# Kernel tuning notes

Measured on AMD Instinct MI355X. Metric: run time of the kernel, lower is better.

## Reference

```python
import jax, jax.numpy as jnp
import numpy as np

B, S, D, F, E, TOP_K = 2, 2048, 1024, 2048, 8, 2


def setup_inputs() -> dict:
    key = jax.random.key(0)
    k0, k1, k2, k3 = jax.random.split(key, 4)
    return {
        "hidden_states": jax.random.normal(k0, (B, S, D), jnp.float32),
        "gate_w": jax.random.normal(k1, (E, D), jnp.float32) * 0.02,   # torch Linear weight [out=E, in=D]
        "w1": jax.random.normal(k2, (E, D, F), jnp.float32) * 0.02,    # per-expert up-proj
        "w2": jax.random.normal(k3, (E, F, D), jnp.float32) * 0.02,    # per-expert down-proj
    }


def reference(hidden_states, gate_w, w1, w2):
    b, s, d = hidden_states.shape
    e = gate_w.shape[0]
    x = hidden_states.reshape(-1, d)                 # [T, D]
    t = x.shape[0]
    router_logits = x @ gate_w.T                     # [T, E]
    # softmax in fp32 as in original, then renormalized top-k weights
    probs = jax.nn.softmax(router_logits.astype(jnp.float32), axis=-1)
    topw, sel = jax.lax.top_k(probs, TOP_K)          # [T, K]
    topw = topw / jnp.sum(topw, axis=-1, keepdims=True)
    topw = topw.astype(x.dtype)
    # dense combine weights: zero for unselected experts (top_k indices are distinct)
    combine = jnp.zeros((t, e), x.dtype).at[jnp.arange(t)[:, None], sel].add(topw)  # [T, E]
    out = jnp.zeros_like(x)
    for ei in range(e):  # small fixed expert count
        h = jax.nn.silu(x @ w1[ei]) @ w2[ei]         # [T, D]
        out = out + combine[:, ei:ei + 1] * h
    return out.reshape(b, s, d), router_logits
```

## Files before the change

### kernel.cpp

```cpp
#include <hip/hip_runtime.h>
#include <hip/hip_bf16.h>
#include <math.h>

#define Tt 4096
#define Dd 1024
#define Ff 2048
#define Ee 8

typedef unsigned short u16;
typedef short bf16x8 __attribute__((ext_vector_type(8)));
typedef float f32x4 __attribute__((ext_vector_type(4)));

__device__ __forceinline__ u16 f2bf(float f) {
  union { float f; unsigned u; } v; v.f = f;
  unsigned r = v.u + 0x7fffu + ((v.u >> 16) & 1u);
  return (u16)(r >> 16);
}

__device__ __forceinline__ void gload16(const void* g, void* l) {
  __builtin_amdgcn_global_load_lds(
      (const __attribute__((address_space(1))) unsigned int*)g,
      (__attribute__((address_space(3))) unsigned int*)l, 16, 0, 0);
}

__device__ __forceinline__ void router_body(
    int t, int tid, const float* __restrict__ x, const float* __restrict__ gw,
    float* __restrict__ logits, u16* __restrict__ xb)
{
  int lane = tid & 63;
  const float* xr = x + (size_t)t * Dd;
  float xv[16];
#pragma unroll
  for (int i = 0; i < 4; ++i) {
    float4 v = *reinterpret_cast<const float4*>(xr + lane * 16 + i * 4);
    xv[i*4+0] = v.x; xv[i*4+1] = v.y; xv[i*4+2] = v.z; xv[i*4+3] = v.w;
  }
  if (xb) {
#pragma unroll
    for (int i = 0; i < 4; ++i) {
      ushort4 b;
      b.x = f2bf(xv[i*4+0]); b.y = f2bf(xv[i*4+1]);
      b.z = f2bf(xv[i*4+2]); b.w = f2bf(xv[i*4+3]);
      *reinterpret_cast<ushort4*>(xb + (size_t)t * Dd + lane * 16 + i * 4) = b;
    }
  }
#pragma unroll
  for (int e = 0; e < Ee; ++e) {
    const float* gr = gw + (size_t)e * Dd + lane * 16;
    float s = 0.f;
#pragma unroll
    for (int i = 0; i < 4; ++i) {
      float4 g = *reinterpret_cast<const float4*>(gr + i * 4);
      s += xv[i*4+0]*g.x + xv[i*4+1]*g.y + xv[i*4+2]*g.z + xv[i*4+3]*g.w;
    }
#pragma unroll
    for (int o = 32; o > 0; o >>= 1) s += __shfl_xor(s, o);
    if (lane == 0) logits[(size_t)t * Ee + e] = s;
  }
}

__device__ __forceinline__ void top2_of(
    const float* __restrict__ logits, int t, int& i1, int& i2, float& wa)
{
  float4 lo = *reinterpret_cast<const float4*>(logits + (size_t)t * 8);
  float4 hi = *reinterpret_cast<const float4*>(logits + (size_t)t * 8 + 4);
  float s[8] = {lo.x, lo.y, lo.z, lo.w, hi.x, hi.y, hi.z, hi.w};
  i1 = 0; float m1 = s[0];
#pragma unroll
  for (int e = 1; e < 8; ++e) if (s[e] > m1) { m1 = s[e]; i1 = e; }
  i2 = -1; float m2 = -__builtin_inff();
#pragma unroll
  for (int e = 0; e < 8; ++e) if (e != i1 && s[e] > m2) { m2 = s[e]; i2 = e; }
  wa = 1.f / (1.f + expf(m2 - m1));
}

__device__ __forceinline__ void transpose_tile(
    const float* __restrict__ ip, u16* __restrict__ op, int R, int C,
    int r0, int c0, int tid, u16 st[][65])
{
  int rr = tid >> 2;
  int cb = (tid & 3) * 16;
#pragma unroll
  for (int i = 0; i < 4; ++i) {
    float4 v = *reinterpret_cast<const float4*>(ip + (size_t)(r0 + rr) * C + c0 + cb + i * 4);
    st[rr][cb + i*4 + 0] = f2bf(v.x);
    st[rr][cb + i*4 + 1] = f2bf(v.y);
    st[rr][cb + i*4 + 2] = f2bf(v.z);
    st[rr][cb + i*4 + 3] = f2bf(v.w);
  }
  __syncthreads();
#pragma unroll
  for (int i = 0; i < 4; ++i) {
    ushort4 b;
    b.x = st[cb + i*4 + 0][rr];
    b.y = st[cb + i*4 + 1][rr];
    b.z = st[cb + i*4 + 2][rr];
    b.w = st[cb + i*4 + 3][rr];
    *reinterpret_cast<ushort4*>(op + (size_t)(c0 + rr) * R + r0 + cb + i * 4) = b;
  }
}

template<int MODE, int N_, int K_>
__device__ __forceinline__ void gemm_body(
    int orig, u16* __restrict__ Al, u16* __restrict__ Bl,
    const u16* __restrict__ Abase, const u16* __restrict__ Bbase,
    void* __restrict__ Cout, const int* __restrict__ meta,
    const int* __restrict__ list, const float* __restrict__ wgt)
{
  constexpr int NXc = N_ / 128;
  constexpr int NYc = 32;
  constexpr int CPX = NXc * NYc;
  constexpr int ABUF = 128 * 32;
  constexpr int NT  = K_ / 32;

  const int swz  = (orig & 7) * CPX + (orig >> 3);
  const int bz   = swz / CPX;
  const int rem  = swz - bz * CPX;
  const int by   = rem / NXc;
  const int bx   = rem - by * NXc;

  const int e   = bz;
  const int cnt = meta[e];
  if (by * 128 >= cnt) return;
  const int off = meta[32 + e];

  const int tid  = threadIdx.x;
  const int lane = tid & 63;
  const int wave = tid >> 6;
  const int wr   = wave >> 1, wc = wave & 1;
  const int n0   = bx * 128;

  const int l4 = lane >> 2;
  const int kp = (((lane & 3) ^ ((lane >> 3) & 3))) * 8;

  const u16* aptr[2];
  int aoff[2];
#pragma unroll
  for (int c = 0; c < 2; ++c) {
    int chunk = wave * 2 + c;
    int row = chunk * 16 + l4;
    int i = by * 128 + row;
    if (i >= cnt) i = cnt - 1;
    int srow = (MODE == 0) ? list[off + i] : (off + i);
    aptr[c] = Abase + (size_t)srow * K_ + kp;
    aoff[c] = chunk * 512;
  }
  const u16* bptr[2];
  int boff[2];
#pragma unroll
  for (int c = 0; c < 2; ++c) {
    int chunk = wave * 2 + c;
    int row = chunk * 16 + l4;
    bptr[c] = Bbase + ((size_t)e * N_ + n0 + row) * K_ + kp;
    boff[c] = chunk * 512;
  }

  f32x4 acc[4][4] = {};
  const int r16 = lane & 15;
  const int kqs = (((lane >> 4) ^ ((lane >> 1) & 3))) * 8;

  u16 *a0 = Al, *a1 = Al + ABUF, *a2 = Al + 2 * ABUF;
  u16 *b0 = Bl, *b1 = Bl + ABUF, *b2 = Bl + 2 * ABUF;

#pragma unroll
  for (int c = 0; c < 2; ++c) { gload16(aptr[c], a0 + aoff[c]); gload16(bptr[c], b0 + boff[c]); }
#pragma unroll
  for (int c = 0; c < 2; ++c) { gload16(aptr[c] + 32, a1 + aoff[c]); gload16(bptr[c] + 32, b1 + boff[c]); }

  for (int t = 0; t < NT; ++t) {
    if (t + 1 < NT) asm volatile("s_waitcnt vmcnt(4)" ::: "memory");
    else            asm volatile("s_waitcnt vmcnt(0)" ::: "memory");
    __builtin_amdgcn_s_barrier();

    if (t + 2 < NT) {
      int k0 = (t + 2) * 32;
#pragma unroll
      for (int c = 0; c < 2; ++c) { gload16(aptr[c] + k0, a2 + aoff[c]); gload16(bptr[c] + k0, b2 + boff[c]); }
    }

    bf16x8 af[4], bfv[4];
#pragma unroll
    for (int m = 0; m < 4; ++m)
      af[m] = *reinterpret_cast<const bf16x8*>(&a0[(wr*64 + m*16 + r16) * 32 + kqs]);
#pragma unroll
    for (int n = 0; n < 4; ++n)
      bfv[n] = *reinterpret_cast<const bf16x8*>(&b0[(wc*64 + n*16 + r16) * 32 + kqs]);
    __builtin_amdgcn_s_setprio(1);
#pragma unroll
    for (int m = 0; m < 4; ++m)
#pragma unroll
      for (int n = 0; n < 4; ++n)
        acc[m][n] = __builtin_amdgcn_mfma_f32_16x16x32_bf16(af[m], bfv[n], acc[m][n], 0, 0, 0);
    __builtin_amdgcn_s_setprio(0);

    u16* ta = a0; a0 = a1; a1 = a2; a2 = ta;
    u16* tb = b0; b0 = b1; b1 = b2; b2 = tb;
  }

  const int colb = n0 + wc * 64 + r16;
  const int rb4  = wr * 64 + ((lane >> 4) << 2);
#pragma unroll
  for (int m = 0; m < 4; ++m) {
#pragma unroll
    for (int r = 0; r < 4; ++r) {
      int i = by * 128 + rb4 + m * 16 + r;
      if (i >= cnt) continue;
      if (MODE == 0) {
        u16* hp = (u16*)Cout + (size_t)(off + i) * N_;
#pragma unroll
        for (int n = 0; n < 4; ++n) {
          float v = acc[m][n][r];
          v = v / (1.f + expf(-v));
          hp[colb + n * 16] = f2bf(v);
        }
      } else {
        int   tok = list[off + i];
        float w   = wgt[off + i];
        float* o = (float*)Cout + (size_t)tok * N_;
#pragma unroll
        for (int n = 0; n < 4; ++n)
          atomicAdd(&o[colb + n * 16], w * acc[m][n][r]);
      }
    }
  }
}

__global__ __launch_bounds__(256) void router_kernel(
    const float* __restrict__ x, const float* __restrict__ gw,
    float* __restrict__ logits, u16* __restrict__ xb)
{
  router_body(blockIdx.x * 4 + (threadIdx.x >> 6), threadIdx.x, x, gw, logits, xb);
}

__global__ __launch_bounds__(256) void fuse1_kernel(
    const float* __restrict__ x, const float* __restrict__ gw,
    float* __restrict__ logits, u16* __restrict__ xb,
    const float* __restrict__ w1, u16* __restrict__ w1T,
    float* __restrict__ outz)
{
  __shared__ u16 st[64][65];
  const int orig = blockIdx.x;
  if (orig < 4096) {
    int swz = (orig & 7) * 512 + (orig >> 3);
    int e   = swz / 512;
    int rem = swz - e * 512;
    int by  = rem / 32, bx = rem - (rem / 32) * 32;
    const size_t eo = (size_t)e * Dd * Ff;
    transpose_tile(w1 + eo, w1T + eo, Dd, Ff, by * 64, bx * 64, threadIdx.x, st);
  } else if (orig < 5120) {
    router_body((orig - 4096) * 4 + (threadIdx.x >> 6), threadIdx.x, x, gw, logits, xb);
  } else {
    int z = orig - 5120;
    float4 zero = make_float4(0.f, 0.f, 0.f, 0.f);
    float4* p = reinterpret_cast<float4*>(outz);
#pragma unroll
    for (int i = 0; i < 16; ++i)
      p[(size_t)z * 4096 + i * 256 + threadIdx.x] = zero;
  }
}

__global__ __launch_bounds__(256) void fuse2_kernel(
    const u16* __restrict__ Abase, const u16* __restrict__ Bbase,
    void* __restrict__ Cout, const int* __restrict__ meta,
    const int* __restrict__ list, const float* __restrict__ wgt,
    const float* __restrict__ w2, u16* __restrict__ w2T)
{
  constexpr int ABUF = 128 * 32;
  __shared__ u16 pool[6 * ABUF];
  const int orig = blockIdx.x;
  if (orig < 4096) {
    gemm_body<0, Ff, Dd>(orig, pool, pool + 3 * ABUF, Abase, Bbase, Cout, meta, list, wgt);
  } else {
    int og  = orig - 4096;
    int swz = (og & 7) * 512 + (og >> 3);
    int e   = swz / 512;
    int rem = swz - e * 512;
    int byy = rem / 16, bxx = rem - (rem / 16) * 16;
    const size_t eo = (size_t)e * Ff * Dd;
    transpose_tile(w2 + eo, w2T + eo, Ff, Dd, byy * 64, bxx * 64, threadIdx.x,
                   reinterpret_cast<u16(*)[65]>(pool));
  }
}

template<int MODE, int N_, int K_>
__global__ __launch_bounds__(256) void gemm_g(
    const u16* __restrict__ Abase, const u16* __restrict__ Bbase,
    void* __restrict__ Cout, const int* __restrict__ meta,
    const int* __restrict__ list, const float* __restrict__ wgt)
{
  constexpr int ABUF = 128 * 32;
  __shared__ u16 Al[3 * ABUF];
  __shared__ u16 Bl[3 * ABUF];
  const int orig = blockIdx.x + (N_ / 128) * (blockIdx.y + 32 * blockIdx.z);
  gemm_body<MODE, N_, K_>(orig, Al, Bl, Abase, Bbase, Cout, meta, list, wgt);
}

__global__ __launch_bounds__(256) void transpose_bf16_kernel(
    const float* __restrict__ in, u16* __restrict__ out, int R, int C)
{
  __shared__ u16 st[64][65];
  const size_t eoff = (size_t)blockIdx.z * R * C;
  transpose_tile(in + eoff, out + eoff, R, C, blockIdx.y * 64, blockIdx.x * 64,
                 threadIdx.x, st);
}

__global__ __launch_bounds__(256) void build1_kernel(
    const float* __restrict__ logits, int* __restrict__ meta)
{
  __shared__ int cnt;
  const int e = blockIdx.x;
  const int tid = threadIdx.x;
  if (tid == 0) cnt = 0;
  __syncthreads();
  int local = 0;
  for (int it = 0; it < Tt / 256; ++it) {
    int t = it * 256 + tid;
    int i1, i2; float wa;
    top2_of(logits, t, i1, i2, wa);
    if (i1 == e || i2 == e) ++local;
  }
  atomicAdd(&cnt, local);
  __syncthreads();
  if (tid == 0) meta[e] = cnt;
}

__global__ __launch_bounds__(256) void build2_kernel(
    const float* __restrict__ logits, int* __restrict__ meta,
    int* __restrict__ list, float* __restrict__ wgt)
{
  __shared__ int cur;
  const int e = blockIdx.x;
  const int tid = threadIdx.x;
  int offv = 0;
  if (tid == 0) {
    for (int g = 0; g < Ee; ++g) { if (g < e) offv += meta[g]; }
    meta[32 + e] = offv;
    cur = 0;
  }
  __syncthreads();
  offv = meta[32 + e];
  for (int it = 0; it < Tt / 256; ++it) {
    int t = it * 256 + tid;
    int i1, i2; float wa;
    top2_of(logits, t, i1, i2, wa);
    float w = (i1 == e) ? wa : ((i2 == e) ? (1.f - wa) : 0.f);
    if (i1 == e || i2 == e) {
      int pos = atomicAdd(&cur, 1);
      list[offv + pos] = t;
      wgt[offv + pos] = w;
    }
  }
}

__global__ __launch_bounds__(256) void combine_kernel(
    const float* __restrict__ logits, float* __restrict__ combine)
{
  int t = blockIdx.x * 256 + threadIdx.x;
  if (t >= Tt) return;
  int i1, i2; float wa;
  top2_of(logits, t, i1, i2, wa);
#pragma unroll
  for (int e = 0; e < 8; ++e)
    combine[(size_t)t * 8 + e] = (e == i1) ? wa : ((e == i2) ? (1.f - wa) : 0.f);
}

template<int MODE, int N_, int K_>
__global__ __launch_bounds__(256) void gemm_dense(
    const float* __restrict__ A, const float* __restrict__ Bg,
    float* __restrict__ C, const float* __restrict__ combine,
    int expert, int first)
{
  constexpr int BM = 128, BN = 128, BK = 32, LDT = 40;
  __shared__ u16 Al[BM * LDT];
  __shared__ u16 Bl[BN * LDT];
  const int tid  = threadIdx.x;
  const int lane = tid & 63;
  const int wave = tid >> 6;
  const int wr = wave >> 1, wc = wave & 1;
  const int m0 = blockIdx.y * BM;
  const int n0 = blockIdx.x * BN;
  f32x4 acc[4][4] = {};
  for (int k0 = 0; k0 < K_; k0 += BK) {
#pragma unroll
    for (int i = 0; i < 4; ++i) {
      int f = tid + 256 * i;
      int row = f >> 3;
      int c4 = (f & 7) << 2;
      float4 v = *reinterpret_cast<const float4*>(A + (size_t)(m0 + row) * K_ + k0 + c4);
      ushort4 b;
      b.x = f2bf(v.x); b.y = f2bf(v.y); b.z = f2bf(v.z); b.w = f2bf(v.w);
      *reinterpret_cast<ushort4*>(&Al[row * LDT + c4]) = b;
    }
    {
      int n  = tid & 127;
      int kb = (tid >> 7) << 4;
      const float* bp = Bg + (size_t)(k0 + kb) * N_ + n0 + n;
      u16 tmp[16];
#pragma unroll
      for (int kk = 0; kk < 16; ++kk)
        tmp[kk] = f2bf(bp[(size_t)kk * N_]);
      u16* p = &Bl[n * LDT + kb];
#pragma unroll
      for (int i = 0; i < 4; ++i) {
        ushort4 b;
        b.x = tmp[i*4+0]; b.y = tmp[i*4+1]; b.z = tmp[i*4+2]; b.w = tmp[i*4+3];
        *reinterpret_cast<ushort4*>(p + i * 4) = b;
      }
    }
    __syncthreads();
    bf16x8 af[4], bfr[4];
    const int kq  = (lane >> 4) << 3;
    const int r16 = lane & 15;
#pragma unroll
    for (int m = 0; m < 4; ++m)
      af[m] = *reinterpret_cast<const bf16x8*>(&Al[(wr*64 + m*16 + r16) * LDT + kq]);
#pragma unroll
    for (int n = 0; n < 4; ++n)
      bfr[n] = *reinterpret_cast<const bf16x8*>(&Bl[(wc*64 + n*16 + r16) * LDT + kq]);
#pragma unroll
    for (int m = 0; m < 4; ++m)
#pragma unroll
      for (int n = 0; n < 4; ++n)
        acc[m][n] = __builtin_amdgcn_mfma_f32_16x16x32_bf16(af[m], bfr[n], acc[m][n], 0, 0, 0);
    __syncthreads();
  }
  const int col0 = n0 + wc * 64 + (lane & 15);
  const int rbs  = m0 + wr * 64 + ((lane >> 4) << 2);
#pragma unroll
  for (int m = 0; m < 4; ++m) {
#pragma unroll
    for (int r = 0; r < 4; ++r) {
      int row = rbs + m * 16 + r;
      if (MODE == 0) {
#pragma unroll
        for (int n = 0; n < 4; ++n) {
          float v = acc[m][n][r];
          v = v / (1.f + expf(-v));
          C[(size_t)row * N_ + col0 + n * 16] = v;
        }
      } else {
        float w = combine[(size_t)row * Ee + expert];
        if (first) {
#pragma unroll
          for (int n = 0; n < 4; ++n)
            C[(size_t)row * N_ + col0 + n * 16] = w * acc[m][n][r];
        } else {
#pragma unroll
          for (int n = 0; n < 4; ++n)
            C[(size_t)row * N_ + col0 + n * 16] += w * acc[m][n][r];
        }
      }
    }
  }
}

extern "C" void kernel_launch(void* const* d_in, const int* in_sizes, int n_in,
                              void* d_out, int out_size, void* d_ws, size_t ws_size,
                              hipStream_t stream)
{
  const float* x  = (const float*)d_in[0];
  const float* gw = (const float*)d_in[1];
  const float* w1 = (const float*)d_in[2];
  const float* w2 = (const float*)d_in[3];
  float* out    = (float*)d_out;
  float* logits = out + (size_t)Tt * Dd;

  int*   meta = (int*)d_ws;
  int*   list = (int*)((char*)d_ws + 256);
  float* wgt  = (float*)((char*)d_ws + 256 + 32768);
  u16*   xb   = (u16*)((char*)d_ws + 262144);
  u16*   h1   = (u16*)((char*)d_ws + 262144 + 8388608);
  u16*   wA   = (u16*)((char*)d_ws + 262144 + 8388608 + 33554432);
  u16*   wB   = (u16*)((char*)d_ws + 262144 + 8388608 + 2*33554432ull);
  const size_t NEED_B = 262144ull + 8388608ull + 33554432ull + 33554432ull;
  const size_t NEED_A = NEED_B + 33554432ull;

  if (ws_size >= NEED_B) {
    fuse1_kernel<<<5376, 256, 0, stream>>>(x, gw, logits, xb, w1, wA, out);
    build1_kernel<<<Ee, 256, 0, stream>>>(logits, meta);
    build2_kernel<<<Ee, 256, 0, stream>>>(logits, meta, list, wgt);
    if (ws_size >= NEED_A) {
      fuse2_kernel<<<8192, 256, 0, stream>>>(xb, wA, h1, meta, list, wgt, w2, wB);
      gemm_g<1, Dd, Ff><<<dim3(Dd/128, 32, 8), 256, 0, stream>>>(h1, wB, out, meta, list, wgt);
    } else {
      gemm_g<0, Ff, Dd><<<dim3(Ff/128, 32, 8), 256, 0, stream>>>(xb, wA, h1, meta, list, wgt);
      transpose_bf16_kernel<<<dim3(Dd/64, Ff/64, Ee), 256, 0, stream>>>(w2, wA, Ff, Dd);
      gemm_g<1, Dd, Ff><<<dim3(Dd/128, 32, 8), 256, 0, stream>>>(h1, wA, out, meta, list, wgt);
    }
  } else {
    float* combine = (float*)d_ws;
    float* h1d     = combine + (size_t)Tt * Ee;
    router_kernel<<<Tt / 4, 256, 0, stream>>>(x, gw, logits, nullptr);
    combine_kernel<<<Tt / 256, 256, 0, stream>>>(logits, combine);
    size_t cb = (size_t)Tt * Ee * sizeof(float);
    size_t avail = ws_size > cb ? (ws_size - cb) : 0;
    long maxrows = (long)(avail / ((size_t)Ff * sizeof(float)));
    int chunk = (maxrows >= Tt) ? Tt : (int)((maxrows / 128) * 128);
    if (chunk < 128) chunk = 128;
    for (int c0 = 0; c0 < Tt; c0 += chunk) {
      int rows = (Tt - c0) < chunk ? (Tt - c0) : chunk;
      for (int e = 0; e < Ee; ++e) {
        gemm_dense<0, Ff, Dd><<<dim3(Ff/128, rows/128), 256, 0, stream>>>(
            x + (size_t)c0 * Dd, w1 + (size_t)e * Dd * Ff, h1d, nullptr, e, 0);
        gemm_dense<1, Dd, Ff><<<dim3(Dd/128, rows/128), 256, 0, stream>>>(
            h1d, w2 + (size_t)e * Ff * Dd, out + (size_t)c0 * Dd,
            combine + (size_t)c0 * Ee, e, (e == 0) ? 1 : 0);
      }
    }
  }
}
```

Measured before the change: 188.7 us.

## Load GEMM B operand directly from global into registers, bypassing LDS

The expert GEMM body no longer stages the B (weight) tile through shared memory. Each wave loads its B fragments straight from global memory into registers and double-buffers them one k-step ahead, while A keeps its triple-buffered LDS pipeline. The wait counts are adjusted to match. This halves LDS per block, which may raise occupancy and removes the LDS reads for B. In exchange, waves that share B columns now each fetch them from global/L2, and only a one-step register prefetch is there to hide global latency.

```diff
diff --git a/kernel.cpp b/kernel.cpp
--- a/kernel.cpp
+++ b/kernel.cpp
@@ -102,7 +102,7 @@
 
 template<int MODE, int N_, int K_>
 __device__ __forceinline__ void gemm_body(
-    int orig, u16* __restrict__ Al, u16* __restrict__ Bl,
+    int orig, u16* __restrict__ Al,
     const u16* __restrict__ Abase, const u16* __restrict__ Bbase,
     void* __restrict__ Cout, const int* __restrict__ meta,
     const int* __restrict__ list, const float* __restrict__ wgt)
@@ -145,56 +145,61 @@
     aptr[c] = Abase + (size_t)srow * K_ + kp;
     aoff[c] = chunk * 512;
   }
-  const u16* bptr[2];
-  int boff[2];
-#pragma unroll
-  for (int c = 0; c < 2; ++c) {
-    int chunk = wave * 2 + c;
-    int row = chunk * 16 + l4;
-    bptr[c] = Bbase + ((size_t)e * N_ + n0 + row) * K_ + kp;
-    boff[c] = chunk * 512;
-  }
+
+  const int r16 = lane & 15;
+  const int kq  = (lane >> 4) * 8;
+  const int kqs = (((lane >> 4) ^ ((lane >> 1) & 3))) * 8;
+
+  const u16* gb[4];
+#pragma unroll
+  for (int n = 0; n < 4; ++n)
+    gb[n] = Bbase + ((size_t)e * N_ + n0 + wc * 64 + n * 16 + r16) * K_ + kq;
 
   f32x4 acc[4][4] = {};
-  const int r16 = lane & 15;
-  const int kqs = (((lane >> 4) ^ ((lane >> 1) & 3))) * 8;
-
   u16 *a0 = Al, *a1 = Al + ABUF, *a2 = Al + 2 * ABUF;
-  u16 *b0 = Bl, *b1 = Bl + ABUF, *b2 = Bl + 2 * ABUF;
-
-#pragma unroll
-  for (int c = 0; c < 2; ++c) { gload16(aptr[c], a0 + aoff[c]); gload16(bptr[c], b0 + boff[c]); }
-#pragma unroll
-  for (int c = 0; c < 2; ++c) { gload16(aptr[c] + 32, a1 + aoff[c]); gload16(bptr[c] + 32, b1 + boff[c]); }
+
+#pragma unroll
+  for (int c = 0; c < 2; ++c) gload16(aptr[c], a0 + aoff[c]);
+#pragma unroll
+  for (int c = 0; c < 2; ++c) gload16(aptr[c] + 32, a1 + aoff[c]);
+  __builtin_amdgcn_sched_barrier(0);
+  bf16x8 bcur[4], bnxt[4];
+#pragma unroll
+  for (int n = 0; n < 4; ++n) bcur[n] = *reinterpret_cast<const bf16x8*>(gb[n]);
 
   for (int t = 0; t < NT; ++t) {
-    if (t + 1 < NT) asm volatile("s_waitcnt vmcnt(4)" ::: "memory");
+    if (t + 1 < NT) asm volatile("s_waitcnt vmcnt(6)" ::: "memory");
     else            asm volatile("s_waitcnt vmcnt(0)" ::: "memory");
     __builtin_amdgcn_s_barrier();
 
     if (t + 2 < NT) {
       int k0 = (t + 2) * 32;
 #pragma unroll
-      for (int c = 0; c < 2; ++c) { gload16(aptr[c] + k0, a2 + aoff[c]); gload16(bptr[c] + k0, b2 + boff[c]); }
-    }
-
-    bf16x8 af[4], bfv[4];
+      for (int c = 0; c < 2; ++c) gload16(aptr[c] + k0, a2 + aoff[c]);
+    }
+    __builtin_amdgcn_sched_barrier(0);
+    if (t + 1 < NT) {
+      int k0 = (t + 1) * 32;
+#pragma unroll
+      for (int n = 0; n < 4; ++n)
+        bnxt[n] = *reinterpret_cast<const bf16x8*>(gb[n] + k0);
+    }
+
+    bf16x8 af[4];
 #pragma unroll
     for (int m = 0; m < 4; ++m)
       af[m] = *reinterpret_cast<const bf16x8*>(&a0[(wr*64 + m*16 + r16) * 32 + kqs]);
-#pragma unroll
-    for (int n = 0; n < 4; ++n)
-      bfv[n] = *reinterpret_cast<const bf16x8*>(&b0[(wc*64 + n*16 + r16) * 32 + kqs]);
     __builtin_amdgcn_s_setprio(1);
 #pragma unroll
     for (int m = 0; m < 4; ++m)
 #pragma unroll
       for (int n = 0; n < 4; ++n)
-        acc[m][n] = __builtin_amdgcn_mfma_f32_16x16x32_bf16(af[m], bfv[n], acc[m][n], 0, 0, 0);
+        acc[m][n] = __builtin_amdgcn_mfma_f32_16x16x32_bf16(af[m], bcur[n], acc[m][n], 0, 0, 0);
     __builtin_amdgcn_s_setprio(0);
 
+#pragma unroll
+    for (int n = 0; n < 4; ++n) bcur[n] = bnxt[n];
     u16* ta = a0; a0 = a1; a1 = a2; a2 = ta;
-    u16* tb = b0; b0 = b1; b1 = b2; b2 = tb;
   }
 
   const int colb = n0 + wc * 64 + r16;
@@ -266,10 +271,10 @@
     const float* __restrict__ w2, u16* __restrict__ w2T)
 {
   constexpr int ABUF = 128 * 32;
-  __shared__ u16 pool[6 * ABUF];
+  __shared__ u16 pool[3 * ABUF];
   const int orig = blockIdx.x;
   if (orig < 4096) {
-    gemm_body<0, Ff, Dd>(orig, pool, pool + 3 * ABUF, Abase, Bbase, Cout, meta, list, wgt);
+    gemm_body<0, Ff, Dd>(orig, pool, Abase, Bbase, Cout, meta, list, wgt);
   } else {
     int og  = orig - 4096;
     int swz = (og & 7) * 512 + (og >> 3);
@@ -290,9 +295,8 @@
 {
   constexpr int ABUF = 128 * 32;
   __shared__ u16 Al[3 * ABUF];
-  __shared__ u16 Bl[3 * ABUF];
   const int orig = blockIdx.x + (N_ / 128) * (blockIdx.y + 32 * blockIdx.z);
-  gemm_body<MODE, N_, K_>(orig, Al, Bl, Abase, Bbase, Cout, meta, list, wgt);
+  gemm_body<MODE, N_, K_>(orig, Al, Abase, Bbase, Cout, meta, list, wgt);
 }
 
 __global__ __launch_bounds__(256) void transpose_bf16_kernel(
```

Result: slower. 294.7 us (+56.2%).
